# Kernel optimization log

Measured on AMD Instinct MI355X. Metric: run time of the kernel, lower is better.

## Reference

```python
import jax, jax.numpy as jnp
import numpy as np

N, D, H, E, K = 8192, 1024, 4096, 8, 2


def setup_inputs() -> dict:
    key = jax.random.key(0)
    ks = jax.random.split(key, 4)
    scaled = lambda k, shp, fan: (jax.random.normal(k, shp, jnp.float32) / np.sqrt(fan).astype(np.float32))
    return {
        "x": jax.random.normal(ks[0], (N, D), jnp.float32),
        "Wg": scaled(ks[1], (D, E), D),
        "bg": jnp.zeros((E,), jnp.float32),
        "W1": scaled(ks[2], (E, D, H), D),
        "b1": jnp.zeros((E, H), jnp.float32),
        "W2": scaled(ks[3], (E, H, D), H),
        "b2": jnp.zeros((E, D), jnp.float32),
    }


def reference(x, Wg, bg, W1, b1, W2, b2):
    # Gating: softmax over experts, top-k selection, renormalize top-k probs.
    gate_probs = jax.nn.softmax(x @ Wg + bg, axis=-1)            # [N, E]
    topk_p, topk_i = jax.lax.top_k(gate_probs, K)                # [N, K]
    topk_p = topk_p / topk_p.sum(axis=-1, keepdims=True)
    onehot = jax.nn.one_hot(topk_i, E, dtype=x.dtype)            # [N, K, E]
    # Per-token combine weight for each expert (0 if expert not in top-k).
    w = (onehot * topk_p[..., None]).sum(axis=1)                 # [N, E]

    out = jnp.zeros_like(x)
    for e in range(E):  # fixed small loop over structurally distinct experts
        h = jax.nn.relu(x @ W1[e] + b1[e])                       # dropout = identity (eval)
        out = out + w[:, e:e + 1] * (h @ W2[e] + b2[e])

    # Load-balancing auxiliary loss.
    importance = gate_probs.sum(axis=0)
    importance = importance / importance.sum()
    load = onehot.sum(axis=(0, 1)) / (x.shape[0] * K)            # [E]
    lb_loss = E * (importance * load).sum()
    return out, lb_loss
```

## Files before the change

kernel.cpp:

```cpp
#include <hip/hip_runtime.h>
#include <hip/hip_bf16.h>
#include <math.h>

#define NTOK 8192
#define DDIM 1024
#define HDIM 4096
#define NEXP 8
#define KTOP 2
#define MAXROWS 17408
#define MAXTILES 136

typedef __bf16 bf16x8 __attribute__((ext_vector_type(8)));
typedef float f32x4 __attribute__((ext_vector_type(4)));

#define GAS __attribute__((address_space(1)))
#define LAS __attribute__((address_space(3)))

__device__ __forceinline__ void async16(const void* g, void* l) {
  __builtin_amdgcn_global_load_lds((GAS void*)g, (LAS void*)l, 16, 0, 0);
}

#define XB_OFF     ((size_t)0)
#define W1T_OFF    (XB_OFF + (size_t)NTOK*DDIM*2)
#define ROWOUT_OFF W1T_OFF
#define W2T_OFF    (W1T_OFF + (size_t)NEXP*DDIM*HDIM*2)
#define HB_OFF     (W2T_OFF + (size_t)NEXP*HDIM*DDIM*2)
#define ROWTOK_OFF (HB_OFF + (size_t)MAXROWS*HDIM*2)
#define ROWW_OFF   (ROWTOK_OFF + (size_t)MAXROWS*4)
#define TOKE_OFF   (ROWW_OFF + (size_t)MAXROWS*4)
#define TOKW_OFF   (TOKE_OFF + (size_t)NTOK*KTOP*4)
#define TOKROW_OFF (TOKW_OFF + (size_t)NTOK*KTOP*4)
#define TILEE_OFF  (TOKROW_OFF + (size_t)NTOK*KTOP*4)
#define CNT_OFF    (TILEE_OFF + (size_t)256*4)
#define POS_OFF    (CNT_OFF + 64)
#define IMP_OFF    (POS_OFF + 64)
#define META_OFF   (IMP_OFF + 64)

__global__ void init_kernel(int* counts, float* importance) {
  if (threadIdx.x < NEXP) { counts[threadIdx.x] = 0; importance[threadIdx.x] = 0.f; }
}

__global__ void cast_x_kernel(const float* __restrict__ src, __hip_bfloat16* __restrict__ dst) {
  size_t i = ((size_t)blockIdx.x * blockDim.x + threadIdx.x) * 4;
  if (i < (size_t)NTOK * DDIM) {
    float4 v = *(const float4*)(src + i);
    dst[i + 0] = __float2bfloat16(v.x);
    dst[i + 1] = __float2bfloat16(v.y);
    dst[i + 2] = __float2bfloat16(v.z);
    dst[i + 3] = __float2bfloat16(v.w);
  }
}

__global__ __launch_bounds__(256) void transpose_cast_kernel(
    const float* __restrict__ src, __hip_bfloat16* __restrict__ dst, int R, int C) {
  __shared__ float tile[64][65];
  const int e = blockIdx.z;
  const float* s = src + (size_t)e * R * C;
  __hip_bfloat16* d = dst + (size_t)e * R * C;
  const int c0 = blockIdx.x * 64, r0 = blockIdx.y * 64;
  const int tc = (threadIdx.x & 15) * 4;
  const int tr = threadIdx.x >> 4;
#pragma unroll
  for (int p = 0; p < 4; ++p) {
    float4 v = *(const float4*)&s[(size_t)(r0 + tr + p * 16) * C + c0 + tc];
    tile[tr + p * 16][tc + 0] = v.x;
    tile[tr + p * 16][tc + 1] = v.y;
    tile[tr + p * 16][tc + 2] = v.z;
    tile[tr + p * 16][tc + 3] = v.w;
  }
  __syncthreads();
  const int oc = threadIdx.x >> 4;
  const int orr = (threadIdx.x & 15) * 4;
#pragma unroll
  for (int p = 0; p < 4; ++p) {
    const int c = oc + p * 16;
    __hip_bfloat16 tmp[4];
    tmp[0] = __float2bfloat16(tile[orr + 0][c]);
    tmp[1] = __float2bfloat16(tile[orr + 1][c]);
    tmp[2] = __float2bfloat16(tile[orr + 2][c]);
    tmp[3] = __float2bfloat16(tile[orr + 3][c]);
    *(ushort4*)&d[(size_t)(c0 + c) * R + r0 + orr] = *(ushort4*)tmp;
  }
}

__global__ __launch_bounds__(256) void gating_kernel(
    const float* __restrict__ x, const float* __restrict__ Wg, const float* __restrict__ bg,
    int* __restrict__ tok_e, float* __restrict__ tok_w,
    int* __restrict__ counts, float* __restrict__ importance) {
  const int tid = threadIdx.x, wid = tid >> 6, lane = tid & 63;
  const int t = blockIdx.x * 32 + wid * 8 + (lane >> 3);
  const int e = lane & 7;
  const float* xr = x + (size_t)t * DDIM;
  double dot = 0.0;
  for (int d = 0; d < DDIM; d += 4) {
    float4 xv = *(const float4*)(xr + d);
    dot += (double)xv.x * (double)Wg[(d + 0) * NEXP + e];
    dot += (double)xv.y * (double)Wg[(d + 1) * NEXP + e];
    dot += (double)xv.z * (double)Wg[(d + 2) * NEXP + e];
    dot += (double)xv.w * (double)Wg[(d + 3) * NEXP + e];
  }
  double logit = dot + (double)bg[e];
  double m = logit;
  for (int off = 1; off < 8; off <<= 1) {
    double o = __shfl_xor(m, off, 64);
    m = o > m ? o : m;
  }
  double p = exp(logit - m);
  double s = p;
  for (int off = 1; off < 8; off <<= 1) s += __shfl_xor(s, off, 64);
  float prob = (float)(p / s);

  __shared__ float imp[NEXP];
  __shared__ int cnt[NEXP];
  if (tid < NEXP) { imp[tid] = 0.f; cnt[tid] = 0; }
  __syncthreads();
  atomicAdd(&imp[e], prob);

  float bp = prob; int be = e;
  for (int off = 1; off < 8; off <<= 1) {
    float op = __shfl_xor(bp, off, 64); int oe = __shfl_xor(be, off, 64);
    if (op > bp || (op == bp && oe < be)) { bp = op; be = oe; }
  }
  float p2 = (e == be) ? -1.f : prob;
  float sp = p2; int se = e;
  for (int off = 1; off < 8; off <<= 1) {
    float op = __shfl_xor(sp, off, 64); int oe = __shfl_xor(se, off, 64);
    if (op > sp || (op == sp && oe < se)) { sp = op; se = oe; }
  }
  if (e == 0) {
    float tsum = bp + sp;
    tok_e[t * 2 + 0] = be; tok_e[t * 2 + 1] = se;
    tok_w[t * 2 + 0] = bp / tsum; tok_w[t * 2 + 1] = sp / tsum;
    atomicAdd(&cnt[be], 1); atomicAdd(&cnt[se], 1);
  }
  __syncthreads();
  if (tid < NEXP) {
    atomicAdd(&counts[tid], cnt[tid]);
    atomicAdd(&importance[tid], imp[tid]);
  }
}

__global__ void offsets_kernel(const int* __restrict__ counts, int* pos, int* tile_expert,
                               int* meta, int* row_token) {
  if (threadIdx.x == 0) {
    int pb = 0, tb = 0;
    for (int e = 0; e < NEXP; e++) {
      pos[e] = pb;
      int tiles = (counts[e] + 127) >> 7;
      for (int tt = 0; tt < tiles; ++tt) tile_expert[tb + tt] = e;
      pb += tiles * 128; tb += tiles;
    }
    meta[0] = tb;
  }
  __syncthreads();
  for (int i = threadIdx.x; i < MAXROWS; i += blockDim.x) row_token[i] = -1;
}

__global__ void scatter_kernel(const int* __restrict__ tok_e, const float* __restrict__ tok_w,
                               int* __restrict__ pos, int* __restrict__ row_token,
                               float* __restrict__ row_weight, int* __restrict__ tok_row) {
  __shared__ int lcnt[NEXP], lbase[NEXP];
  const int t = blockIdx.x * 256 + threadIdx.x;
  if (threadIdx.x < NEXP) lcnt[threadIdx.x] = 0;
  __syncthreads();
  const int e0 = tok_e[t * 2 + 0], e1 = tok_e[t * 2 + 1];
  const int s0 = atomicAdd(&lcnt[e0], 1);
  const int s1 = atomicAdd(&lcnt[e1], 1);
  __syncthreads();
  if (threadIdx.x < NEXP) lbase[threadIdx.x] = atomicAdd(&pos[threadIdx.x], lcnt[threadIdx.x]);
  __syncthreads();
  int r0 = lbase[e0] + s0; row_token[r0] = t; row_weight[r0] = tok_w[t * 2 + 0]; tok_row[t * 2 + 0] = r0;
  int r1 = lbase[e1] + s1; row_token[r1] = t; row_weight[r1] = tok_w[t * 2 + 1]; tok_row[t * 2 + 1] = r1;
}

__global__ __launch_bounds__(256) void gemm1_kernel(
    const __hip_bfloat16* __restrict__ xb, const __hip_bfloat16* __restrict__ w1t,
    const float* __restrict__ b1, __hip_bfloat16* __restrict__ hb,
    const int* __restrict__ row_token, const int* __restrict__ tile_expert,
    const int* __restrict__ meta) {
  const int tile_y = blockIdx.y;
  if (tile_y >= meta[0]) return;
  const int n0 = blockIdx.x * 128;
  const int e = tile_expert[tile_y];
  const int r0 = tile_y * 128;
  const int tid = threadIdx.x;
  const int wid = tid >> 6, lane = tid & 63;

  __shared__ __align__(16) __hip_bfloat16 As[2][128 * 32];
  __shared__ __align__(16) __hip_bfloat16 Bs[2][128 * 32];

  const int srow = wid * 32 + (lane >> 2);
  const int g = ((lane & 3) ^ (srow & 3)) * 8;
  int t0 = row_token[r0 + srow];      if (t0 < 0) t0 = 0;
  int t1 = row_token[r0 + srow + 16]; if (t1 < 0) t1 = 0;
  const __hip_bfloat16* ga0 = xb + (size_t)t0 * DDIM + g;
  const __hip_bfloat16* ga1 = xb + (size_t)t1 * DDIM + g;
  const __hip_bfloat16* gb0 = w1t + ((size_t)e * HDIM + n0 + srow) * DDIM + g;
  const __hip_bfloat16* gb1 = gb0 + (size_t)16 * DDIM;
  const int ldsA0 = (wid * 32) * 32, ldsA1 = (wid * 32 + 16) * 32;

  f32x4 acc[4][4] = {};
  const int wm = (wid & 1) * 64, wn = (wid >> 1) * 64;
  const int fr = lane & 15;
  const int soff = ((lane >> 4) ^ (lane & 3)) * 8;

#define STAGE1(b) do { \
    async16(ga0, &As[b][ldsA0]); async16(ga1, &As[b][ldsA1]); \
    async16(gb0, &Bs[b][ldsA0]); async16(gb1, &Bs[b][ldsA1]); \
    ga0 += 32; ga1 += 32; gb0 += 32; gb1 += 32; } while (0)

  STAGE1(0);
  for (int kt = 0; kt < DDIM / 32; ++kt) {
    const int cur = kt & 1;
    __syncthreads();
    if (kt + 1 < DDIM / 32) { if (cur) STAGE1(0); else STAGE1(1); }
    bf16x8 av[4], bv[4];
#pragma unroll
    for (int i = 0; i < 4; i++) av[i] = *(const bf16x8*)&As[cur][(wm + i * 16 + fr) * 32 + soff];
#pragma unroll
    for (int j = 0; j < 4; j++) bv[j] = *(const bf16x8*)&Bs[cur][(wn + j * 16 + fr) * 32 + soff];
#pragma unroll
    for (int i = 0; i < 4; i++)
#pragma unroll
      for (int j = 0; j < 4; j++)
        acc[i][j] = __builtin_amdgcn_mfma_f32_16x16x32_bf16(av[i], bv[j], acc[i][j], 0, 0, 0);
  }
#undef STAGE1

  const int crow = (lane >> 4) * 4;
  const int ccol = lane & 15;
#pragma unroll
  for (int j = 0; j < 4; j++) {
    const int gc = n0 + wn + j * 16 + ccol;
    const float bias = b1[e * HDIM + gc];
#pragma unroll
    for (int i = 0; i < 4; i++) {
      const int grb = r0 + wm + i * 16 + crow;
#pragma unroll
      for (int r = 0; r < 4; r++) {
        float v = acc[i][j][r] + bias;
        v = v > 0.f ? v : 0.f;
        hb[(size_t)(grb + r) * HDIM + gc] = __float2bfloat16(v);
      }
    }
  }
}

__global__ __launch_bounds__(256) void gemm2_kernel(
    const __hip_bfloat16* __restrict__ hb, const __hip_bfloat16* __restrict__ w2t,
    const float* __restrict__ b2, __hip_bfloat16* __restrict__ rowout,
    const int* __restrict__ tile_expert, const int* __restrict__ meta) {
  const int tile_y = blockIdx.x % MAXTILES;
  const int cx = blockIdx.x / MAXTILES;
  if (tile_y >= meta[0]) return;
  const int n0 = cx * 128;
  const int e = tile_expert[tile_y];
  const int r0 = tile_y * 128;
  const int tid = threadIdx.x;
  const int wid = tid >> 6, lane = tid & 63;

  __shared__ __align__(16) __hip_bfloat16 As[2][128 * 32];
  __shared__ __align__(16) __hip_bfloat16 Bs[2][128 * 32];

  const int srow = wid * 32 + (lane >> 2);
  const int g = ((lane & 3) ^ (srow & 3)) * 8;
  const __hip_bfloat16* ga0 = hb + ((size_t)r0 + srow) * HDIM + g;
  const __hip_bfloat16* ga1 = ga0 + (size_t)16 * HDIM;
  const __hip_bfloat16* gb0 = w2t + ((size_t)e * DDIM + n0 + srow) * HDIM + g;
  const __hip_bfloat16* gb1 = gb0 + (size_t)16 * HDIM;
  const int ldsA0 = (wid * 32) * 32, ldsA1 = (wid * 32 + 16) * 32;

  f32x4 acc[4][4] = {};
  const int wm = (wid & 1) * 64, wn = (wid >> 1) * 64;
  const int fr = lane & 15;
  const int soff = ((lane >> 4) ^ (lane & 3)) * 8;

#define STAGE2(b) do { \
    async16(ga0, &As[b][ldsA0]); async16(ga1, &As[b][ldsA1]); \
    async16(gb0, &Bs[b][ldsA0]); async16(gb1, &Bs[b][ldsA1]); \
    ga0 += 32; ga1 += 32; gb0 += 32; gb1 += 32; } while (0)

  STAGE2(0);
  for (int kt = 0; kt < HDIM / 32; ++kt) {
    const int cur = kt & 1;
    __syncthreads();
    if (kt + 1 < HDIM / 32) { if (cur) STAGE2(0); else STAGE2(1); }
    bf16x8 av[4], bv[4];
#pragma unroll
    for (int i = 0; i < 4; i++) av[i] = *(const bf16x8*)&As[cur][(wm + i * 16 + fr) * 32 + soff];
#pragma unroll
    for (int j = 0; j < 4; j++) bv[j] = *(const bf16x8*)&Bs[cur][(wn + j * 16 + fr) * 32 + soff];
#pragma unroll
    for (int i = 0; i < 4; i++)
#pragma unroll
      for (int j = 0; j < 4; j++)
        acc[i][j] = __builtin_amdgcn_mfma_f32_16x16x32_bf16(av[i], bv[j], acc[i][j], 0, 0, 0);
  }
#undef STAGE2

  const int crow = (lane >> 4) * 4;
  const int ccol = lane & 15;
#pragma unroll
  for (int j = 0; j < 4; j++) {
    const int gc = n0 + wn + j * 16 + ccol;
    const float bias = b2[e * DDIM + gc];
#pragma unroll
    for (int i = 0; i < 4; i++) {
      const int rr = r0 + wm + i * 16 + crow;
#pragma unroll
      for (int r = 0; r < 4; r++)
        rowout[(size_t)(rr + r) * DDIM + gc] = __float2bfloat16(acc[i][j][r] + bias);
    }
  }
}

__global__ __launch_bounds__(256) void combine_kernel(
    const __hip_bfloat16* __restrict__ rowout, const int* __restrict__ tok_row,
    const float* __restrict__ row_weight, float* __restrict__ out) {
  const int idx = blockIdx.x * 256 + threadIdx.x;
  const int t = idx >> 7;
  const int d = (idx & 127) * 8;
  const int r0 = tok_row[t * 2 + 0], r1 = tok_row[t * 2 + 1];
  const float w0 = row_weight[r0], w1 = row_weight[r1];
  bf16x8 a = *(const bf16x8*)&rowout[(size_t)r0 * DDIM + d];
  bf16x8 b = *(const bf16x8*)&rowout[(size_t)r1 * DDIM + d];
  float o[8];
#pragma unroll
  for (int k = 0; k < 8; k++) o[k] = w0 * (float)a[k] + w1 * (float)b[k];
  float* dst = out + (size_t)t * DDIM + d;
  *(float4*)(dst + 0) = make_float4(o[0], o[1], o[2], o[3]);
  *(float4*)(dst + 4) = make_float4(o[4], o[5], o[6], o[7]);
}

__global__ void finalize_kernel(const float* __restrict__ importance,
                                const int* __restrict__ counts, float* __restrict__ lb_out) {
  if (threadIdx.x == 0 && blockIdx.x == 0) {
    float s = 0.f;
    for (int e = 0; e < NEXP; e++) s += importance[e];
    float lb = 0.f;
    for (int e = 0; e < NEXP; e++)
      lb += (importance[e] / s) * ((float)counts[e] / (float)(NTOK * KTOP));
    lb_out[0] = (float)NEXP * lb;
  }
}

extern "C" void kernel_launch(void* const* d_in, const int* in_sizes, int n_in,
                              void* d_out, int out_size, void* d_ws, size_t ws_size,
                              hipStream_t stream) {
  (void)in_sizes; (void)n_in; (void)out_size; (void)ws_size;
  const float* x  = (const float*)d_in[0];
  const float* Wg = (const float*)d_in[1];
  const float* bg = (const float*)d_in[2];
  const float* W1 = (const float*)d_in[3];
  const float* b1 = (const float*)d_in[4];
  const float* W2 = (const float*)d_in[5];
  const float* b2 = (const float*)d_in[6];
  float* out = (float*)d_out;

  char* ws = (char*)d_ws;
  __hip_bfloat16* xb     = (__hip_bfloat16*)(ws + XB_OFF);
  __hip_bfloat16* w1t    = (__hip_bfloat16*)(ws + W1T_OFF);
  __hip_bfloat16* rowout = (__hip_bfloat16*)(ws + ROWOUT_OFF);
  __hip_bfloat16* w2t    = (__hip_bfloat16*)(ws + W2T_OFF);
  __hip_bfloat16* hb     = (__hip_bfloat16*)(ws + HB_OFF);
  int*   row_token  = (int*)(ws + ROWTOK_OFF);
  float* row_weight = (float*)(ws + ROWW_OFF);
  int*   tok_e   = (int*)(ws + TOKE_OFF);
  float* tok_w   = (float*)(ws + TOKW_OFF);
  int*   tok_row = (int*)(ws + TOKROW_OFF);
  int*   tile_e  = (int*)(ws + TILEE_OFF);
  int*   counts  = (int*)(ws + CNT_OFF);
  int*   pos     = (int*)(ws + POS_OFF);
  float* importance = (float*)(ws + IMP_OFF);
  int*   meta    = (int*)(ws + META_OFF);

  init_kernel<<<1, 64, 0, stream>>>(counts, importance);
  cast_x_kernel<<<NTOK * DDIM / 4 / 256, 256, 0, stream>>>(x, xb);
  transpose_cast_kernel<<<dim3(HDIM / 64, DDIM / 64, NEXP), 256, 0, stream>>>(W1, w1t, DDIM, HDIM);
  transpose_cast_kernel<<<dim3(DDIM / 64, HDIM / 64, NEXP), 256, 0, stream>>>(W2, w2t, HDIM, DDIM);
  gating_kernel<<<NTOK / 32, 256, 0, stream>>>(x, Wg, bg, tok_e, tok_w, counts, importance);
  offsets_kernel<<<1, 256, 0, stream>>>(counts, pos, tile_e, meta, row_token);
  scatter_kernel<<<NTOK / 256, 256, 0, stream>>>(tok_e, tok_w, pos, row_token, row_weight, tok_row);
  gemm1_kernel<<<dim3(HDIM / 128, MAXTILES), 256, 0, stream>>>(xb, w1t, b1, hb, row_token, tile_e, meta);
  gemm2_kernel<<<dim3((DDIM / 128) * MAXTILES), 256, 0, stream>>>(hb, w2t, b2, rowout, tile_e, meta);
  combine_kernel<<<NTOK * 128 / 256, 256, 0, stream>>>(rowout, tok_row, row_weight, out);
  finalize_kernel<<<1, 64, 0, stream>>>(importance, counts, out + (size_t)NTOK * DDIM);
}
```

Baseline: 818.8 us.

## Preshuffle expert weights into MFMA fragment order and load B directly to registers

```diff
diff --git a/kernel.cpp b/kernel.cpp
--- a/kernel.cpp
+++ b/kernel.cpp
@@ -21,10 +21,10 @@
 }
 
 #define XB_OFF     ((size_t)0)
-#define W1T_OFF    (XB_OFF + (size_t)NTOK*DDIM*2)
-#define ROWOUT_OFF W1T_OFF
-#define W2T_OFF    (W1T_OFF + (size_t)NEXP*DDIM*HDIM*2)
-#define HB_OFF     (W2T_OFF + (size_t)NEXP*HDIM*DDIM*2)
+#define W1S_OFF    (XB_OFF + (size_t)NTOK*DDIM*2)
+#define ROWOUT_OFF W1S_OFF
+#define W2S_OFF    (W1S_OFF + (size_t)NEXP*DDIM*HDIM*2)
+#define HB_OFF     (W2S_OFF + (size_t)NEXP*HDIM*DDIM*2)
 #define ROWTOK_OFF (HB_OFF + (size_t)MAXROWS*HDIM*2)
 #define ROWW_OFF   (ROWTOK_OFF + (size_t)MAXROWS*4)
 #define TOKE_OFF   (ROWW_OFF + (size_t)MAXROWS*4)
@@ -51,36 +51,27 @@
   }
 }
 
-__global__ __launch_bounds__(256) void transpose_cast_kernel(
-    const float* __restrict__ src, __hip_bfloat16* __restrict__ dst, int R, int C) {
-  __shared__ float tile[64][65];
-  const int e = blockIdx.z;
-  const float* s = src + (size_t)e * R * C;
-  __hip_bfloat16* d = dst + (size_t)e * R * C;
-  const int c0 = blockIdx.x * 64, r0 = blockIdx.y * 64;
-  const int tc = (threadIdx.x & 15) * 4;
-  const int tr = threadIdx.x >> 4;
-#pragma unroll
-  for (int p = 0; p < 4; ++p) {
-    float4 v = *(const float4*)&s[(size_t)(r0 + tr + p * 16) * C + c0 + tc];
-    tile[tr + p * 16][tc + 0] = v.x;
-    tile[tr + p * 16][tc + 1] = v.y;
-    tile[tr + p * 16][tc + 2] = v.z;
-    tile[tr + p * 16][tc + 3] = v.w;
-  }
-  __syncthreads();
-  const int oc = threadIdx.x >> 4;
-  const int orr = (threadIdx.x & 15) * 4;
-#pragma unroll
-  for (int p = 0; p < 4; ++p) {
-    const int c = oc + p * 16;
-    __hip_bfloat16 tmp[4];
-    tmp[0] = __float2bfloat16(tile[orr + 0][c]);
-    tmp[1] = __float2bfloat16(tile[orr + 1][c]);
-    tmp[2] = __float2bfloat16(tile[orr + 2][c]);
-    tmp[3] = __float2bfloat16(tile[orr + 3][c]);
-    *(ushort4*)&d[(size_t)(c0 + c) * R + r0 + orr] = *(ushort4*)tmp;
-  }
+__global__ __launch_bounds__(256) void preshuffle_kernel(
+    const float* __restrict__ src, __hip_bfloat16* __restrict__ dst, int K, int N) {
+  __shared__ float t[32][33];
+  const int e = blockIdx.z, nb2 = blockIdx.y, kb = blockIdx.x;
+  const float* s = src + (size_t)e * K * N + (size_t)kb * 32 * N + nb2 * 32;
+  const int r = threadIdx.x >> 3, c4 = (threadIdx.x & 7) * 4;
+  float4 v = *(const float4*)&s[(size_t)r * N + c4];
+  t[r][c4 + 0] = v.x; t[r][c4 + 1] = v.y; t[r][c4 + 2] = v.z; t[r][c4 + 3] = v.w;
+  __syncthreads();
+  const int h = threadIdx.x >> 7;
+  const int f = (threadIdx.x & 127) * 4;
+  const int lane = f >> 3, j0 = f & 7;
+  const int n = (lane & 15) + h * 16, kq = (lane >> 4) * 8;
+  __hip_bfloat16 o[4];
+  o[0] = __float2bfloat16(t[kq + j0 + 0][n]);
+  o[1] = __float2bfloat16(t[kq + j0 + 1][n]);
+  o[2] = __float2bfloat16(t[kq + j0 + 2][n]);
+  o[3] = __float2bfloat16(t[kq + j0 + 3][n]);
+  const size_t nb = (size_t)nb2 * 2 + h;
+  __hip_bfloat16* d = dst + (((size_t)e * (N / 16) + nb) * (K / 32) + kb) * 512 + f;
+  *(ushort4*)d = *(ushort4*)o;
 }
 
 __global__ __launch_bounds__(256) void gating_kernel(
@@ -174,7 +165,7 @@
 }
 
 __global__ __launch_bounds__(256) void gemm1_kernel(
-    const __hip_bfloat16* __restrict__ xb, const __hip_bfloat16* __restrict__ w1t,
+    const __hip_bfloat16* __restrict__ xb, const __hip_bfloat16* __restrict__ w1s,
     const float* __restrict__ b1, __hip_bfloat16* __restrict__ hb,
     const int* __restrict__ row_token, const int* __restrict__ tile_expert,
     const int* __restrict__ meta) {
@@ -183,49 +174,68 @@
   const int n0 = blockIdx.x * 128;
   const int e = tile_expert[tile_y];
   const int r0 = tile_y * 128;
-  const int tid = threadIdx.x;
-  const int wid = tid >> 6, lane = tid & 63;
+  const int tid = threadIdx.x, wid = tid >> 6, lane = tid & 63;
 
   __shared__ __align__(16) __hip_bfloat16 As[2][128 * 32];
-  __shared__ __align__(16) __hip_bfloat16 Bs[2][128 * 32];
 
   const int srow = wid * 32 + (lane >> 2);
-  const int g = ((lane & 3) ^ (srow & 3)) * 8;
+  const int g = ((lane & 3) ^ ((lane >> 3) & 3)) * 8;
   int t0 = row_token[r0 + srow];      if (t0 < 0) t0 = 0;
   int t1 = row_token[r0 + srow + 16]; if (t1 < 0) t1 = 0;
   const __hip_bfloat16* ga0 = xb + (size_t)t0 * DDIM + g;
   const __hip_bfloat16* ga1 = xb + (size_t)t1 * DDIM + g;
-  const __hip_bfloat16* gb0 = w1t + ((size_t)e * HDIM + n0 + srow) * DDIM + g;
-  const __hip_bfloat16* gb1 = gb0 + (size_t)16 * DDIM;
   const int ldsA0 = (wid * 32) * 32, ldsA1 = (wid * 32 + 16) * 32;
 
+  const int wm = (wid & 1) * 64, wn = (wid >> 1) * 64;
+  const __hip_bfloat16* bp[4];
+#pragma unroll
+  for (int j = 0; j < 4; j++) {
+    const size_t nb = (size_t)(n0 + wn) / 16 + j;
+    bp[j] = w1s + ((size_t)e * (HDIM / 16) + nb) * (DDIM / 32) * 512 + lane * 8;
+  }
+
   f32x4 acc[4][4] = {};
-  const int wm = (wid & 1) * 64, wn = (wid >> 1) * 64;
   const int fr = lane & 15;
-  const int soff = ((lane >> 4) ^ (lane & 3)) * 8;
-
-#define STAGE1(b) do { \
-    async16(ga0, &As[b][ldsA0]); async16(ga1, &As[b][ldsA1]); \
-    async16(gb0, &Bs[b][ldsA0]); async16(gb1, &Bs[b][ldsA1]); \
-    ga0 += 32; ga1 += 32; gb0 += 32; gb1 += 32; } while (0)
-
-  STAGE1(0);
-  for (int kt = 0; kt < DDIM / 32; ++kt) {
-    const int cur = kt & 1;
+  const int soff = ((lane >> 4) ^ ((lane >> 1) & 3)) * 8;
+
+  bf16x8 bv0[4], bv1[4];
+  async16(ga0, &As[0][ldsA0]); async16(ga1, &As[0][ldsA1]); ga0 += 32; ga1 += 32;
+#pragma unroll
+  for (int j = 0; j < 4; j++) { bv0[j] = *(const bf16x8*)bp[j]; bp[j] += 512; }
+
+  const int NK = DDIM / 32;
+  for (int kt = 0; kt < NK; kt += 2) {
     __syncthreads();
-    if (kt + 1 < DDIM / 32) { if (cur) STAGE1(0); else STAGE1(1); }
-    bf16x8 av[4], bv[4];
-#pragma unroll
-    for (int i = 0; i < 4; i++) av[i] = *(const bf16x8*)&As[cur][(wm + i * 16 + fr) * 32 + soff];
-#pragma unroll
-    for (int j = 0; j < 4; j++) bv[j] = *(const bf16x8*)&Bs[cur][(wn + j * 16 + fr) * 32 + soff];
-#pragma unroll
-    for (int i = 0; i < 4; i++)
-#pragma unroll
-      for (int j = 0; j < 4; j++)
-        acc[i][j] = __builtin_amdgcn_mfma_f32_16x16x32_bf16(av[i], bv[j], acc[i][j], 0, 0, 0);
-  }
-#undef STAGE1
+    async16(ga0, &As[1][ldsA0]); async16(ga1, &As[1][ldsA1]); ga0 += 32; ga1 += 32;
+#pragma unroll
+    for (int j = 0; j < 4; j++) { bv1[j] = *(const bf16x8*)bp[j]; bp[j] += 512; }
+    {
+      bf16x8 av[4];
+#pragma unroll
+      for (int i = 0; i < 4; i++) av[i] = *(const bf16x8*)&As[0][(wm + i * 16 + fr) * 32 + soff];
+#pragma unroll
+      for (int i = 0; i < 4; i++)
+#pragma unroll
+        for (int j = 0; j < 4; j++)
+          acc[i][j] = __builtin_amdgcn_mfma_f32_16x16x32_bf16(av[i], bv0[j], acc[i][j], 0, 0, 0);
+    }
+    __syncthreads();
+    if (kt + 2 < NK) {
+      async16(ga0, &As[0][ldsA0]); async16(ga1, &As[0][ldsA1]); ga0 += 32; ga1 += 32;
+#pragma unroll
+      for (int j = 0; j < 4; j++) { bv0[j] = *(const bf16x8*)bp[j]; bp[j] += 512; }
+    }
+    {
+      bf16x8 av[4];
+#pragma unroll
+      for (int i = 0; i < 4; i++) av[i] = *(const bf16x8*)&As[1][(wm + i * 16 + fr) * 32 + soff];
+#pragma unroll
+      for (int i = 0; i < 4; i++)
+#pragma unroll
+        for (int j = 0; j < 4; j++)
+          acc[i][j] = __builtin_amdgcn_mfma_f32_16x16x32_bf16(av[i], bv1[j], acc[i][j], 0, 0, 0);
+    }
+  }
 
   const int crow = (lane >> 4) * 4;
   const int ccol = lane & 15;
@@ -247,56 +257,74 @@
 }
 
 __global__ __launch_bounds__(256) void gemm2_kernel(
-    const __hip_bfloat16* __restrict__ hb, const __hip_bfloat16* __restrict__ w2t,
+    const __hip_bfloat16* __restrict__ hb, const __hip_bfloat16* __restrict__ w2s,
     const float* __restrict__ b2, __hip_bfloat16* __restrict__ rowout,
     const int* __restrict__ tile_expert, const int* __restrict__ meta) {
-  const int tile_y = blockIdx.x % MAXTILES;
-  const int cx = blockIdx.x / MAXTILES;
+  const int tile_y = blockIdx.y;
   if (tile_y >= meta[0]) return;
-  const int n0 = cx * 128;
+  const int n0 = blockIdx.x * 128;
   const int e = tile_expert[tile_y];
   const int r0 = tile_y * 128;
-  const int tid = threadIdx.x;
-  const int wid = tid >> 6, lane = tid & 63;
+  const int tid = threadIdx.x, wid = tid >> 6, lane = tid & 63;
 
   __shared__ __align__(16) __hip_bfloat16 As[2][128 * 32];
-  __shared__ __align__(16) __hip_bfloat16 Bs[2][128 * 32];
 
   const int srow = wid * 32 + (lane >> 2);
-  const int g = ((lane & 3) ^ (srow & 3)) * 8;
+  const int g = ((lane & 3) ^ ((lane >> 3) & 3)) * 8;
   const __hip_bfloat16* ga0 = hb + ((size_t)r0 + srow) * HDIM + g;
   const __hip_bfloat16* ga1 = ga0 + (size_t)16 * HDIM;
-  const __hip_bfloat16* gb0 = w2t + ((size_t)e * DDIM + n0 + srow) * HDIM + g;
-  const __hip_bfloat16* gb1 = gb0 + (size_t)16 * HDIM;
   const int ldsA0 = (wid * 32) * 32, ldsA1 = (wid * 32 + 16) * 32;
 
+  const int wm = (wid & 1) * 64, wn = (wid >> 1) * 64;
+  const __hip_bfloat16* bp[4];
+#pragma unroll
+  for (int j = 0; j < 4; j++) {
+    const size_t nb = (size_t)(n0 + wn) / 16 + j;
+    bp[j] = w2s + ((size_t)e * (DDIM / 16) + nb) * (HDIM / 32) * 512 + lane * 8;
+  }
+
   f32x4 acc[4][4] = {};
-  const int wm = (wid & 1) * 64, wn = (wid >> 1) * 64;
   const int fr = lane & 15;
-  const int soff = ((lane >> 4) ^ (lane & 3)) * 8;
-
-#define STAGE2(b) do { \
-    async16(ga0, &As[b][ldsA0]); async16(ga1, &As[b][ldsA1]); \
-    async16(gb0, &Bs[b][ldsA0]); async16(gb1, &Bs[b][ldsA1]); \
-    ga0 += 32; ga1 += 32; gb0 += 32; gb1 += 32; } while (0)
-
-  STAGE2(0);
-  for (int kt = 0; kt < HDIM / 32; ++kt) {
-    const int cur = kt & 1;
+  const int soff = ((lane >> 4) ^ ((lane >> 1) & 3)) * 8;
+
+  bf16x8 bv0[4], bv1[4];
+  async16(ga0, &As[0][ldsA0]); async16(ga1, &As[0][ldsA1]); ga0 += 32; ga1 += 32;
+#pragma unroll
+  for (int j = 0; j < 4; j++) { bv0[j] = *(const bf16x8*)bp[j]; bp[j] += 512; }
+
+  const int NK = HDIM / 32;
+  for (int kt = 0; kt < NK; kt += 2) {
     __syncthreads();
-    if (kt + 1 < HDIM / 32) { if (cur) STAGE2(0); else STAGE2(1); }
-    bf16x8 av[4], bv[4];
-#pragma unroll
-    for (int i = 0; i < 4; i++) av[i] = *(const bf16x8*)&As[cur][(wm + i * 16 + fr) * 32 + soff];
-#pragma unroll
-    for (int j = 0; j < 4; j++) bv[j] = *(const bf16x8*)&Bs[cur][(wn + j * 16 + fr) * 32 + soff];
-#pragma unroll
-    for (int i = 0; i < 4; i++)
-#pragma unroll
-      for (int j = 0; j < 4; j++)
-        acc[i][j] = __builtin_amdgcn_mfma_f32_16x16x32_bf16(av[i], bv[j], acc[i][j], 0, 0, 0);
-  }
-#undef STAGE2
+    async16(ga0, &As[1][ldsA0]); async16(ga1, &As[1][ldsA1]); ga0 += 32; ga1 += 32;
+#pragma unroll
+    for (int j = 0; j < 4; j++) { bv1[j] = *(const bf16x8*)bp[j]; bp[j] += 512; }
+    {
+      bf16x8 av[4];
+#pragma unroll
+      for (int i = 0; i < 4; i++) av[i] = *(const bf16x8*)&As[0][(wm + i * 16 + fr) * 32 + soff];
+#pragma unroll
+      for (int i = 0; i < 4; i++)
+#pragma unroll
+        for (int j = 0; j < 4; j++)
+          acc[i][j] = __builtin_amdgcn_mfma_f32_16x16x32_bf16(av[i], bv0[j], acc[i][j], 0, 0, 0);
+    }
+    __syncthreads();
+    if (kt + 2 < NK) {
+      async16(ga0, &As[0][ldsA0]); async16(ga1, &As[0][ldsA1]); ga0 += 32; ga1 += 32;
+#pragma unroll
+      for (int j = 0; j < 4; j++) { bv0[j] = *(const bf16x8*)bp[j]; bp[j] += 512; }
+    }
+    {
+      bf16x8 av[4];
+#pragma unroll
+      for (int i = 0; i < 4; i++) av[i] = *(const bf16x8*)&As[1][(wm + i * 16 + fr) * 32 + soff];
+#pragma unroll
+      for (int i = 0; i < 4; i++)
+#pragma unroll
+        for (int j = 0; j < 4; j++)
+          acc[i][j] = __builtin_amdgcn_mfma_f32_16x16x32_bf16(av[i], bv1[j], acc[i][j], 0, 0, 0);
+    }
+  }
 
   const int crow = (lane >> 4) * 4;
   const int ccol = lane & 15;
@@ -359,9 +387,9 @@
 
   char* ws = (char*)d_ws;
   __hip_bfloat16* xb     = (__hip_bfloat16*)(ws + XB_OFF);
-  __hip_bfloat16* w1t    = (__hip_bfloat16*)(ws + W1T_OFF);
+  __hip_bfloat16* w1s    = (__hip_bfloat16*)(ws + W1S_OFF);
   __hip_bfloat16* rowout = (__hip_bfloat16*)(ws + ROWOUT_OFF);
-  __hip_bfloat16* w2t    = (__hip_bfloat16*)(ws + W2T_OFF);
+  __hip_bfloat16* w2s    = (__hip_bfloat16*)(ws + W2S_OFF);
   __hip_bfloat16* hb     = (__hip_bfloat16*)(ws + HB_OFF);
   int*   row_token  = (int*)(ws + ROWTOK_OFF);
   float* row_weight = (float*)(ws + ROWW_OFF);
@@ -376,13 +404,13 @@
 
   init_kernel<<<1, 64, 0, stream>>>(counts, importance);
   cast_x_kernel<<<NTOK * DDIM / 4 / 256, 256, 0, stream>>>(x, xb);
-  transpose_cast_kernel<<<dim3(HDIM / 64, DDIM / 64, NEXP), 256, 0, stream>>>(W1, w1t, DDIM, HDIM);
-  transpose_cast_kernel<<<dim3(DDIM / 64, HDIM / 64, NEXP), 256, 0, stream>>>(W2, w2t, HDIM, DDIM);
+  preshuffle_kernel<<<dim3(DDIM / 32, HDIM / 32, NEXP), 256, 0, stream>>>(W1, w1s, DDIM, HDIM);
+  preshuffle_kernel<<<dim3(HDIM / 32, DDIM / 32, NEXP), 256, 0, stream>>>(W2, w2s, HDIM, DDIM);
   gating_kernel<<<NTOK / 32, 256, 0, stream>>>(x, Wg, bg, tok_e, tok_w, counts, importance);
   offsets_kernel<<<1, 256, 0, stream>>>(counts, pos, tile_e, meta, row_token);
   scatter_kernel<<<NTOK / 256, 256, 0, stream>>>(tok_e, tok_w, pos, row_token, row_weight, tok_row);
-  gemm1_kernel<<<dim3(HDIM / 128, MAXTILES), 256, 0, stream>>>(xb, w1t, b1, hb, row_token, tile_e, meta);
-  gemm2_kernel<<<dim3((DDIM / 128) * MAXTILES), 256, 0, stream>>>(hb, w2t, b2, rowout, tile_e, meta);
+  gemm1_kernel<<<dim3(HDIM / 128, MAXTILES), 256, 0, stream>>>(xb, w1s, b1, hb, row_token, tile_e, meta);
+  gemm2_kernel<<<dim3(DDIM / 128, MAXTILES), 256, 0, stream>>>(hb, w2s, b2, rowout, tile_e, meta);
   combine_kernel<<<NTOK * 128 / 256, 256, 0, stream>>>(rowout, tok_row, row_weight, out);
   finalize_kernel<<<1, 64, 0, stream>>>(importance, counts, out + (size_t)NTOK * DDIM);
 }
```

Result: slower. 921.9 us (+12.6%).
